# Performance work log

Measured on AMD Instinct MI355X. Metric: run time of the kernel, lower is better.

The kernel has to match this reference:

```python
import jax, jax.numpy as jnp
import numpy as np

QUERY_DIM = 1024
KEY_DIM = 768
NUM_HEADS = 16
HEAD_DIM = QUERY_DIM // NUM_HEADS


def _linear_params(key, in_dim, out_dim):
    kw, kb = jax.random.split(key)
    bound = 1.0 / np.sqrt(in_dim)
    W = jax.random.uniform(kw, (out_dim, in_dim), minval=-bound, maxval=bound, dtype=jnp.float32)
    b = jax.random.uniform(kb, (out_dim,), minval=-bound, maxval=bound, dtype=jnp.float32)
    return W, b


def setup_inputs() -> dict:
    key = jax.random.key(0)
    ks = jax.random.split(key, 7)
    B, Nq, Nk = 4, 1024, 2048
    query = jax.random.normal(ks[0], (B, Nq, QUERY_DIM), dtype=jnp.float32)
    k_in = jax.random.normal(ks[1], (B, Nk, KEY_DIM), dtype=jnp.float32)
    v_in = jax.random.normal(ks[2], (B, Nk, KEY_DIM), dtype=jnp.float32)
    Wq, bq = _linear_params(ks[3], QUERY_DIM, QUERY_DIM)
    Wk, bk = _linear_params(ks[4], KEY_DIM, QUERY_DIM)
    Wv, bv = _linear_params(ks[5], KEY_DIM, QUERY_DIM)
    Wo, bo = _linear_params(ks[6], QUERY_DIM, QUERY_DIM)
    return {
        "query": query, "key": k_in, "value": v_in,
        "Wq": Wq, "bq": bq, "Wk": Wk, "bk": bk,
        "Wv": Wv, "bv": bv, "Wo": Wo, "bo": bo,
    }


def reference(query, key, value, Wq, bq, Wk, bk, Wv, bv, Wo, bo):
    B, Nq, _ = query.shape
    Nk = key.shape[1]
    H, D = NUM_HEADS, HEAD_DIM
    scale = 1.0 / np.sqrt(D)
    # Projections (torch Linear: x @ W.T + b), then split heads -> (B, H, N, D)
    Q = (query @ Wq.T + bq).reshape(B, Nq, H, D).transpose(0, 2, 1, 3)
    K = (key @ Wk.T + bk).reshape(B, Nk, H, D).transpose(0, 2, 1, 3)
    V = (value @ Wv.T + bv).reshape(B, Nk, H, D).transpose(0, 2, 1, 3)
    # Explicit score matrix (B, H, Nq, Nk), softmax over keys
    attn = jnp.einsum('bhqd,bhkd->bhqk', Q, K) * scale
    attn = jax.nn.softmax(attn, axis=-1)
    out = jnp.einsum('bhqk,bhkd->bhqd', attn, V)
    out = out.transpose(0, 2, 1, 3).reshape(B, Nq, H * D)
    return out @ Wo.T + bo
```

## Files before the change

kernel.cpp:

```cpp
#include <hip/hip_runtime.h>
#include <stdint.h>


typedef __attribute__((ext_vector_type(4))) float f32x4;
typedef __attribute__((ext_vector_type(8))) _Float16 half8;
typedef __attribute__((ext_vector_type(4))) _Float16 half4;
typedef __attribute__((ext_vector_type(4))) short short4v;
typedef unsigned short u16;

__device__ __forceinline__ u16 f2h(float f){
  _Float16 h = (_Float16)f;
  return __builtin_bit_cast(unsigned short, h);
}

__device__ __forceinline__ void gload16(const void* g, void* lds){
  __builtin_amdgcn_global_load_lds((const __attribute__((address_space(1))) void*)g,
                                   (__attribute__((address_space(3))) void*)lds, 16, 0, 0);
}

struct Seg { const float* s; u16* d; int n4; };
struct Cvt7 { Seg seg[7]; };

__global__ __launch_bounds__(256) void cvt_f32_f16(Cvt7 a){
  Seg sg = a.seg[blockIdx.y];
  const long stride = (long)gridDim.x * 256;
  for (long i = (long)blockIdx.x*256 + threadIdx.x; i < sg.n4; i += stride){
    f32x4 v = *(const f32x4*)(sg.s + i*4);
    short4v h;
    h[0] = (short)f2h(v[0]); h[1] = (short)f2h(v[1]);
    h[2] = (short)f2h(v[2]); h[3] = (short)f2h(v[3]);
    *(short4v*)(sg.d + i*4) = h;
  }
}

template<int R>
__device__ __forceinline__ void stage_tile(const char* gbase, long gstride, char* lds, int tid){
  const int w = tid >> 6, lane = tid & 63;
  #pragma unroll
  for (int it = 0; it < R/32; ++it){
    int c  = (it*4 + w)*64 + lane;
    int r  = c >> 3;
    int bs = (c & 7) << 4;
    int sb = bs ^ ((r & 7) << 4);
    gload16(gbase + (long)r*gstride + sb, lds + (it*4 + w)*1024);
  }
}

template<int LAYOUT>
__global__ __launch_bounds__(256, 2)
void gemm_bt(const u16* __restrict__ A, const u16* __restrict__ Bt,
             const float* __restrict__ bias, u16* __restrict__ out16,
             float* __restrict__ outF, int K, int logS, float scale, int NkT)
{
  __shared__ __align__(128) char Alds[16384];
  __shared__ __align__(128) char Blds[16384];
  const int tid = threadIdx.x, lane = tid & 63, w = tid >> 6;
  const int g = lane >> 4, lm = lane & 15;
  const int row0 = blockIdx.x * 128, col0 = blockIdx.y * 128;
  const int wr = (w >> 1) * 64, wc = (w & 1) * 64;

  f32x4 acc[4][4];
  #pragma unroll
  for (int i = 0; i < 4; ++i)
    #pragma unroll
    for (int j = 0; j < 4; ++j) acc[i][j] = {0.f, 0.f, 0.f, 0.f};

  const char* Ag = (const char*)A  + ((long)row0 * K) * 2;
  const char* Bg = (const char*)Bt + ((long)col0 * K) * 2;

  for (int k0 = 0; k0 < K; k0 += 64){
    stage_tile<128>(Ag + k0*2, (long)K*2, Alds, tid);
    stage_tile<128>(Bg + k0*2, (long)K*2, Blds, tid);
    __syncthreads();
    #pragma unroll
    for (int kk = 0; kk < 2; ++kk){
      half8 af[4], bfr[4];
      #pragma unroll
      for (int mi = 0; mi < 4; ++mi){
        int r = wr + mi*16 + lm;
        af[mi] = *(const half8*)(Alds + r*128 + ((kk*64 + g*16) ^ ((r & 7) << 4)));
      }
      #pragma unroll
      for (int ni = 0; ni < 4; ++ni){
        int r = wc + ni*16 + lm;
        bfr[ni] = *(const half8*)(Blds + r*128 + ((kk*64 + g*16) ^ ((r & 7) << 4)));
      }
      #pragma unroll
      for (int mi = 0; mi < 4; ++mi)
        #pragma unroll
        for (int ni = 0; ni < 4; ++ni)
          acc[mi][ni] = __builtin_amdgcn_mfma_f32_16x16x32_f16(af[mi], bfr[ni], acc[mi][ni], 0, 0, 0);
    }
    __syncthreads();
  }

  float bv[4];
  #pragma unroll
  for (int ni = 0; ni < 4; ++ni) bv[ni] = bias[col0 + wc + ni*16 + lm];
  #pragma unroll
  for (int mi = 0; mi < 4; ++mi){
    #pragma unroll
    for (int ni = 0; ni < 4; ++ni){
      int n = col0 + wc + ni*16 + lm;
      #pragma unroll
      for (int r = 0; r < 4; ++r){
        int m = row0 + wr + mi*16 + g*4 + r;
        float v = (acc[mi][ni][r] + bv[ni]) * scale;
        if (LAYOUT == 3){
          outF[(long)m * 1024 + n] = v;
        } else {
          int b_ = m >> logS, s_ = m & ((1 << logS) - 1);
          int h_ = n >> 6,    d_ = n & 63;
          long dst;
          if (LAYOUT == 1) dst = (((long)(b_*16 + h_) << logS) + s_) * 64 + d_;
          else             dst = ((long)(b_*16 + h_) * 64 + d_) * (long)NkT + s_;
          out16[dst] = f2h(v);
        }
      }
    }
  }
}

__global__ __launch_bounds__(256, 2)
void attn_fused(const u16* __restrict__ Qw, const u16* __restrict__ Kw,
                const u16* __restrict__ Vtw, u16* __restrict__ AO)
{
  __shared__ __align__(128) char Klds[8192];
  __shared__ __align__(128) char Vlds[8192];
  const int tid = threadIdx.x, lane = tid & 63, w = tid >> 6;
  const int g = lane >> 4, lm = lane & 15;
  const int qt = blockIdx.x, bh = blockIdx.y;
  const long qbase = (long)bh * 1024 * 64;
  const long kbase = (long)bh * 2048 * 64;
  const long vbase = (long)bh * 64 * 2048;

  const int q0[2] = { qt*128 + w*32, qt*128 + w*32 + 16 };
  half8 aQ[2][2];
  #pragma unroll
  for (int s = 0; s < 2; ++s)
    #pragma unroll
    for (int kk = 0; kk < 2; ++kk)
      aQ[s][kk] = *(const half8*)((const char*)Qw + (qbase + (long)(q0[s] + lm)*64 + kk*32 + g*8)*2);

  float mrun[2] = {-3e38f, -3e38f};
  float lrun[2] = {0.f, 0.f};
  f32x4 O[2][4];
  #pragma unroll
  for (int s = 0; s < 2; ++s)
    #pragma unroll
    for (int di = 0; di < 4; ++di) O[s][di] = {0.f, 0.f, 0.f, 0.f};

  for (int kt = 0; kt < 2048; kt += 64){
    stage_tile<64>((const char*)Kw  + (kbase + (long)kt*64)*2, 128,  Klds, tid);
    stage_tile<64>((const char*)Vtw + (vbase + kt)*2,          4096, Vlds, tid);
    __syncthreads();

    half8 kf[4][2];
    #pragma unroll
    for (int t = 0; t < 4; ++t)
      #pragma unroll
      for (int kk = 0; kk < 2; ++kk){
        int r = t*16 + lm;
        kf[t][kk] = *(const half8*)(Klds + r*128 + ((kk*64 + g*16) ^ ((r & 7) << 4)));
      }

    #pragma unroll
    for (int s = 0; s < 2; ++s){
      f32x4 sc[4];
      #pragma unroll
      for (int t = 0; t < 4; ++t){
        f32x4 z = {0.f, 0.f, 0.f, 0.f};
        z = __builtin_amdgcn_mfma_f32_16x16x32_f16(kf[t][0], aQ[s][0], z, 0, 0, 0);
        z = __builtin_amdgcn_mfma_f32_16x16x32_f16(kf[t][1], aQ[s][1], z, 0, 0, 0);
        sc[t] = z;
      }
      float pm = sc[0][0];
      #pragma unroll
      for (int t = 0; t < 4; ++t)
        #pragma unroll
        for (int r = 0; r < 4; ++r) pm = fmaxf(pm, sc[t][r]);
      pm = fmaxf(pm, __shfl_xor(pm, 16));
      pm = fmaxf(pm, __shfl_xor(pm, 32));
      float mnew = fmaxf(mrun[s], pm);
      float fac  = __expf(mrun[s] - mnew);
      float ls = 0.f;
      #pragma unroll
      for (int t = 0; t < 4; ++t)
        #pragma unroll
        for (int r = 0; r < 4; ++r){ float p = __expf(sc[t][r] - mnew); sc[t][r] = p; ls += p; }
      ls += __shfl_xor(ls, 16);
      ls += __shfl_xor(ls, 32);
      lrun[s] = lrun[s]*fac + ls;
      mrun[s] = mnew;
      float frow[4];
      #pragma unroll
      for (int r = 0; r < 4; ++r) frow[r] = __shfl(fac, (lane & 48) | (g*4 + r));
      #pragma unroll
      for (int di = 0; di < 4; ++di){
        O[s][di][0] *= frow[0]; O[s][di][1] *= frow[1];
        O[s][di][2] *= frow[2]; O[s][di][3] *= frow[3];
      }
      half8 pa[2];
      #pragma unroll
      for (int kh = 0; kh < 2; ++kh)
        #pragma unroll
        for (int i = 0; i < 8; ++i){
          int t = kh*2 + (i >> 2), r = i & 3;
          pa[kh][i] = (_Float16)sc[t][r];
        }
      #pragma unroll
      for (int di = 0; di < 4; ++di){
        int d = di*16 + lm;
        int swz = (d & 7) << 4;
        #pragma unroll
        for (int kh = 0; kh < 2; ++kh){
          half4 lo = *(const half4*)(Vlds + d*128 + ((kh*64 + g*8)      ^ swz));
          half4 hi = *(const half4*)(Vlds + d*128 + ((kh*64 + g*8 + 32) ^ swz));
          half8 vf = { lo[0], lo[1], lo[2], lo[3], hi[0], hi[1], hi[2], hi[3] };
          O[s][di] = __builtin_amdgcn_mfma_f32_16x16x32_f16(pa[kh], vf, O[s][di], 0, 0, 0);
        }
      }
    }
    __syncthreads();
  }

  const int b = bh >> 4, h = bh & 15;
  #pragma unroll
  for (int s = 0; s < 2; ++s){
    float inv = 1.f / lrun[s];
    float irow[4];
    #pragma unroll
    for (int r = 0; r < 4; ++r) irow[r] = __shfl(inv, (lane & 48) | (g*4 + r));
    #pragma unroll
    for (int di = 0; di < 4; ++di)
      #pragma unroll
      for (int r = 0; r < 4; ++r){
        long q = q0[s] + g*4 + r;
        AO[((long)b*1024 + q)*1024 + h*64 + di*16 + lm] = f2h(O[s][di][r] * irow[r]);
      }
  }
}

extern "C" void kernel_launch(void* const* d_in, const int* in_sizes, int n_in,
                              void* d_out, int out_size, void* d_ws, size_t ws_size,
                              hipStream_t stream)
{
  const float* query = (const float*)d_in[0];
  const float* key   = (const float*)d_in[1];
  const float* value = (const float*)d_in[2];
  const float* Wq = (const float*)d_in[3];
  const float* bq = (const float*)d_in[4];
  const float* Wk = (const float*)d_in[5];
  const float* bk = (const float*)d_in[6];
  const float* Wv = (const float*)d_in[7];
  const float* bv = (const float*)d_in[8];
  const float* Wo = (const float*)d_in[9];
  const float* bo = (const float*)d_in[10];
  float* out = (float*)d_out;

  char* p = (char*)d_ws;
  auto alloc = [&](long bytes){ char* r = p; p += bytes; return r; };
  u16* qH  = (u16*)alloc( 8l<<20);
  u16* kH  = (u16*)alloc(12l<<20);
  u16* vH  = (u16*)alloc(12l<<20);
  u16* WqH = (u16*)alloc( 2l<<20);
  u16* WkH = (u16*)alloc( 2l<<20);
  u16* WvH = (u16*)alloc( 2l<<20);
  u16* WoH = (u16*)alloc( 2l<<20);
  u16* Qw  = (u16*)alloc( 8l<<20);
  u16* Kw  = (u16*)alloc(16l<<20);
  u16* Vtw = (u16*)alloc(16l<<20);
  u16* AO  = (u16*)alloc( 8l<<20);

  Cvt7 ca;
  ca.seg[0] = { query, qH,  4096*1024/4 };
  ca.seg[1] = { key,   kH,  8192*768/4  };
  ca.seg[2] = { value, vH,  8192*768/4  };
  ca.seg[3] = { Wq,    WqH, 1024*1024/4 };
  ca.seg[4] = { Wk,    WkH, 1024*768/4  };
  ca.seg[5] = { Wv,    WvH, 1024*768/4  };
  ca.seg[6] = { Wo,    WoH, 1024*1024/4 };
  cvt_f32_f16<<<dim3(512, 7), 256, 0, stream>>>(ca);

  dim3 blk(256);
  gemm_bt<1><<<dim3(32, 8), blk, 0, stream>>>(qH, WqH, bq, Qw,  nullptr, 1024, 10, 0.125f, 2048);
  gemm_bt<1><<<dim3(64, 8), blk, 0, stream>>>(kH, WkH, bk, Kw,  nullptr,  768, 11, 1.0f,   2048);
  gemm_bt<2><<<dim3(64, 8), blk, 0, stream>>>(vH, WvH, bv, Vtw, nullptr,  768, 11, 1.0f,   2048);
  attn_fused<<<dim3(8, 64), blk, 0, stream>>>(Qw, Kw, Vtw, AO);
  gemm_bt<3><<<dim3(32, 8), blk, 0, stream>>>(AO, WoH, bo, nullptr, out, 1024, 10, 1.0f, 2048);
}
```

Measured before the change: 278.7 us.

## Merge QKV projections into one launch, shrink GEMM tiles, widen attention blocks

Fuses the three Q/K/V projection GEMMs into a single kernel launch with 64x128 tiles, so each GEMM gets more blocks and more blocks can reside per CU. The V-transpose output is staged through LDS and written as 16-byte vectors instead of scattered 2-byte stores. The attention kernel now uses 512 threads with one 16-row query strip per wave, and the grid is remapped so blocks sharing a head are grouped. Each staged K/V tile is now shared by eight waves, but every wave does less work per tile, and the smaller GEMM tiles reload more operand data per output.

```diff
diff --git a/kernel.cpp b/kernel.cpp
--- a/kernel.cpp
+++ b/kernel.cpp
@@ -6,6 +6,7 @@
 typedef __attribute__((ext_vector_type(8))) _Float16 half8;
 typedef __attribute__((ext_vector_type(4))) _Float16 half4;
 typedef __attribute__((ext_vector_type(4))) short short4v;
+typedef __attribute__((ext_vector_type(8))) short short8;
 typedef unsigned short u16;
 
 __device__ __forceinline__ u16 f2h(float f){
@@ -33,95 +34,127 @@
   }
 }
 
-template<int R>
+template<int R, int THREADS>
 __device__ __forceinline__ void stage_tile(const char* gbase, long gstride, char* lds, int tid){
   const int w = tid >> 6, lane = tid & 63;
   #pragma unroll
-  for (int it = 0; it < R/32; ++it){
-    int c  = (it*4 + w)*64 + lane;
+  for (int it = 0; it < R*8/THREADS; ++it){
+    int c  = it*THREADS + w*64 + lane;
     int r  = c >> 3;
     int bs = (c & 7) << 4;
     int sb = bs ^ ((r & 7) << 4);
-    gload16(gbase + (long)r*gstride + sb, lds + (it*4 + w)*1024);
-  }
-}
-
-template<int LAYOUT>
-__global__ __launch_bounds__(256, 2)
-void gemm_bt(const u16* __restrict__ A, const u16* __restrict__ Bt,
-             const float* __restrict__ bias, u16* __restrict__ out16,
-             float* __restrict__ outF, int K, int logS, float scale, int NkT)
+    gload16(gbase + (long)r*gstride + sb, lds + (it*THREADS + w*64)*16);
+  }
+}
+
+__device__ __forceinline__ void gemm64_mainloop(const u16* A, const u16* Bt, int K,
+                                                int row0, int col0, int tid,
+                                                char* Alds, char* Blds, f32x4 acc[2][4]){
+  const int lane = tid & 63, w = tid >> 6;
+  const int g = lane >> 4, lm = lane & 15;
+  const int wr = (w >> 1) * 32, wc = (w & 1) * 64;
+  const char* Ag = (const char*)A  + ((long)row0 * K) * 2;
+  const char* Bg = (const char*)Bt + ((long)col0 * K) * 2;
+  for (int k0 = 0; k0 < K; k0 += 64){
+    stage_tile<64, 256>(Ag + k0*2, (long)K*2, Alds, tid);
+    stage_tile<128, 256>(Bg + k0*2, (long)K*2, Blds, tid);
+    __syncthreads();
+    #pragma unroll
+    for (int kk = 0; kk < 2; ++kk){
+      half8 af[2], bfr[4];
+      #pragma unroll
+      for (int mi = 0; mi < 2; ++mi){
+        int r = wr + mi*16 + lm;
+        af[mi] = *(const half8*)(Alds + r*128 + ((kk*64 + g*16) ^ ((r & 7) << 4)));
+      }
+      #pragma unroll
+      for (int ni = 0; ni < 4; ++ni){
+        int r = wc + ni*16 + lm;
+        bfr[ni] = *(const half8*)(Blds + r*128 + ((kk*64 + g*16) ^ ((r & 7) << 4)));
+      }
+      #pragma unroll
+      for (int mi = 0; mi < 2; ++mi)
+        #pragma unroll
+        for (int ni = 0; ni < 4; ++ni)
+          acc[mi][ni] = __builtin_amdgcn_mfma_f32_16x16x32_f16(af[mi], bfr[ni], acc[mi][ni], 0, 0, 0);
+    }
+    __syncthreads();
+  }
+}
+
+__global__ __launch_bounds__(256, 4)
+void qkv_proj(const u16* __restrict__ qH, const u16* __restrict__ kH, const u16* __restrict__ vH,
+              const u16* __restrict__ WqH, const u16* __restrict__ WkH, const u16* __restrict__ WvH,
+              const float* __restrict__ bq, const float* __restrict__ bk, const float* __restrict__ bv,
+              u16* __restrict__ Qw, u16* __restrict__ Kw, u16* __restrict__ Vtw)
 {
-  __shared__ __align__(128) char Alds[16384];
+  __shared__ __align__(128) char Alds[8192];
   __shared__ __align__(128) char Blds[16384];
   const int tid = threadIdx.x, lane = tid & 63, w = tid >> 6;
   const int g = lane >> 4, lm = lane & 15;
-  const int row0 = blockIdx.x * 128, col0 = blockIdx.y * 128;
-  const int wr = (w >> 1) * 64, wc = (w & 1) * 64;
-
-  f32x4 acc[4][4];
-  #pragma unroll
-  for (int i = 0; i < 4; ++i)
+
+  int bid = blockIdx.x;
+  const u16 *A, *Bt; const float* bias; u16* out16;
+  int K, logS, local; float scale = 1.0f;
+  int which;
+  if (bid < 512)       { which = 0; local = bid;        A = qH; Bt = WqH; bias = bq; out16 = Qw;  K = 1024; logS = 10; scale = 0.125f; }
+  else if (bid < 1536) { which = 1; local = bid - 512;  A = kH; Bt = WkH; bias = bk; out16 = Kw;  K = 768;  logS = 11; }
+  else                 { which = 2; local = bid - 1536; A = vH; Bt = WvH; bias = bv; out16 = Vtw; K = 768;  logS = 11; }
+  const int rb = local >> 3, cb = local & 7;
+  const int row0 = rb * 64, col0 = cb * 128;
+
+  f32x4 acc[2][4];
+  #pragma unroll
+  for (int i = 0; i < 2; ++i)
     #pragma unroll
     for (int j = 0; j < 4; ++j) acc[i][j] = {0.f, 0.f, 0.f, 0.f};
 
-  const char* Ag = (const char*)A  + ((long)row0 * K) * 2;
-  const char* Bg = (const char*)Bt + ((long)col0 * K) * 2;
-
-  for (int k0 = 0; k0 < K; k0 += 64){
-    stage_tile<128>(Ag + k0*2, (long)K*2, Alds, tid);
-    stage_tile<128>(Bg + k0*2, (long)K*2, Blds, tid);
-    __syncthreads();
-    #pragma unroll
-    for (int kk = 0; kk < 2; ++kk){
-      half8 af[4], bfr[4];
-      #pragma unroll
-      for (int mi = 0; mi < 4; ++mi){
-        int r = wr + mi*16 + lm;
-        af[mi] = *(const half8*)(Alds + r*128 + ((kk*64 + g*16) ^ ((r & 7) << 4)));
-      }
+  gemm64_mainloop(A, Bt, K, row0, col0, tid, Alds, Blds, acc);
+
+  const int wr = (w >> 1) * 32, wc = (w & 1) * 64;
+  if (which != 2){
+    #pragma unroll
+    for (int mi = 0; mi < 2; ++mi)
       #pragma unroll
       for (int ni = 0; ni < 4; ++ni){
-        int r = wc + ni*16 + lm;
-        bfr[ni] = *(const half8*)(Blds + r*128 + ((kk*64 + g*16) ^ ((r & 7) << 4)));
-      }
-      #pragma unroll
-      for (int mi = 0; mi < 4; ++mi)
+        int n = col0 + wc + ni*16 + lm;
+        float bvv = bias[n];
+        int h_ = n >> 6, d_ = n & 63;
         #pragma unroll
-        for (int ni = 0; ni < 4; ++ni)
-          acc[mi][ni] = __builtin_amdgcn_mfma_f32_16x16x32_f16(af[mi], bfr[ni], acc[mi][ni], 0, 0, 0);
-    }
-    __syncthreads();
-  }
-
-  float bv[4];
-  #pragma unroll
-  for (int ni = 0; ni < 4; ++ni) bv[ni] = bias[col0 + wc + ni*16 + lm];
-  #pragma unroll
-  for (int mi = 0; mi < 4; ++mi){
-    #pragma unroll
-    for (int ni = 0; ni < 4; ++ni){
-      int n = col0 + wc + ni*16 + lm;
-      #pragma unroll
-      for (int r = 0; r < 4; ++r){
-        int m = row0 + wr + mi*16 + g*4 + r;
-        float v = (acc[mi][ni][r] + bv[ni]) * scale;
-        if (LAYOUT == 3){
-          outF[(long)m * 1024 + n] = v;
-        } else {
+        for (int r = 0; r < 4; ++r){
+          int m = row0 + wr + mi*16 + g*4 + r;
           int b_ = m >> logS, s_ = m & ((1 << logS) - 1);
-          int h_ = n >> 6,    d_ = n & 63;
-          long dst;
-          if (LAYOUT == 1) dst = (((long)(b_*16 + h_) << logS) + s_) * 64 + d_;
-          else             dst = ((long)(b_*16 + h_) * 64 + d_) * (long)NkT + s_;
-          out16[dst] = f2h(v);
+          long dst = (((long)(b_*16 + h_) << logS) + s_) * 64 + d_;
+          out16[dst] = f2h((acc[mi][ni][r] + bvv) * scale);
         }
       }
-    }
-  }
-}
-
-__global__ __launch_bounds__(256, 2)
+  } else {
+    #pragma unroll
+    for (int mi = 0; mi < 2; ++mi)
+      #pragma unroll
+      for (int ni = 0; ni < 4; ++ni){
+        int np = wc + ni*16 + lm;
+        float bvv = bias[col0 + np];
+        short4v h4;
+        #pragma unroll
+        for (int r = 0; r < 4; ++r) h4[r] = (short)f2h(acc[mi][ni][r] + bvv);
+        int mb = (wr + mi*16 + g*4) * 2;
+        *(short4v*)(Blds + np*128 + (mb ^ ((np & 7) << 4))) = h4;
+      }
+    __syncthreads();
+    const int b_ = row0 >> 11;
+    #pragma unroll
+    for (int pass = 0; pass < 4; ++pass){
+      int idx = pass*256 + tid, row = idx >> 3, c = idx & 7;
+      short8 v = *(const short8*)(Blds + row*128 + ((c*16) ^ ((row & 7) << 4)));
+      int ng = col0 + row, h_ = ng >> 6, d_ = ng & 63;
+      long dst = ((long)(b_*16 + h_)*64 + d_)*2048 + (row0 & 2047) + c*8;
+      *(short8*)(out16 + dst) = v;
+    }
+  }
+}
+
+__global__ __launch_bounds__(512, 4)
 void attn_fused(const u16* __restrict__ Qw, const u16* __restrict__ Kw,
                 const u16* __restrict__ Vtw, u16* __restrict__ AO)
 {
@@ -129,30 +162,28 @@
   __shared__ __align__(128) char Vlds[8192];
   const int tid = threadIdx.x, lane = tid & 63, w = tid >> 6;
   const int g = lane >> 4, lm = lane & 15;
-  const int qt = blockIdx.x, bh = blockIdx.y;
+  const int p = blockIdx.x;
+  const int slot = p >> 3;
+  const int bh = (p & 7) + ((slot & 7) << 3);
+  const int qt = slot >> 3;
   const long qbase = (long)bh * 1024 * 64;
   const long kbase = (long)bh * 2048 * 64;
   const long vbase = (long)bh * 64 * 2048;
 
-  const int q0[2] = { qt*128 + w*32, qt*128 + w*32 + 16 };
-  half8 aQ[2][2];
-  #pragma unroll
-  for (int s = 0; s < 2; ++s)
-    #pragma unroll
-    for (int kk = 0; kk < 2; ++kk)
-      aQ[s][kk] = *(const half8*)((const char*)Qw + (qbase + (long)(q0[s] + lm)*64 + kk*32 + g*8)*2);
-
-  float mrun[2] = {-3e38f, -3e38f};
-  float lrun[2] = {0.f, 0.f};
-  f32x4 O[2][4];
-  #pragma unroll
-  for (int s = 0; s < 2; ++s)
-    #pragma unroll
-    for (int di = 0; di < 4; ++di) O[s][di] = {0.f, 0.f, 0.f, 0.f};
+  const int q0 = qt*128 + w*16;
+  half8 aQ[2];
+  #pragma unroll
+  for (int kk = 0; kk < 2; ++kk)
+    aQ[kk] = *(const half8*)((const char*)Qw + (qbase + (long)(q0 + lm)*64 + kk*32 + g*8)*2);
+
+  float mrun = -3e38f, lrun = 0.f;
+  f32x4 O[4];
+  #pragma unroll
+  for (int di = 0; di < 4; ++di) O[di] = {0.f, 0.f, 0.f, 0.f};
 
   for (int kt = 0; kt < 2048; kt += 64){
-    stage_tile<64>((const char*)Kw  + (kbase + (long)kt*64)*2, 128,  Klds, tid);
-    stage_tile<64>((const char*)Vtw + (vbase + kt)*2,          4096, Vlds, tid);
+    stage_tile<64, 512>((const char*)Kw  + (kbase + (long)kt*64)*2, 128,  Klds, tid);
+    stage_tile<64, 512>((const char*)Vtw + (vbase + kt)*2,          4096, Vlds, tid);
     __syncthreads();
 
     half8 kf[4][2];
@@ -164,81 +195,109 @@
         kf[t][kk] = *(const half8*)(Klds + r*128 + ((kk*64 + g*16) ^ ((r & 7) << 4)));
       }
 
-    #pragma unroll
-    for (int s = 0; s < 2; ++s){
-      f32x4 sc[4];
-      #pragma unroll
-      for (int t = 0; t < 4; ++t){
-        f32x4 z = {0.f, 0.f, 0.f, 0.f};
-        z = __builtin_amdgcn_mfma_f32_16x16x32_f16(kf[t][0], aQ[s][0], z, 0, 0, 0);
-        z = __builtin_amdgcn_mfma_f32_16x16x32_f16(kf[t][1], aQ[s][1], z, 0, 0, 0);
-        sc[t] = z;
-      }
-      float pm = sc[0][0];
-      #pragma unroll
-      for (int t = 0; t < 4; ++t)
-        #pragma unroll
-        for (int r = 0; r < 4; ++r) pm = fmaxf(pm, sc[t][r]);
-      pm = fmaxf(pm, __shfl_xor(pm, 16));
-      pm = fmaxf(pm, __shfl_xor(pm, 32));
-      float mnew = fmaxf(mrun[s], pm);
-      float fac  = __expf(mrun[s] - mnew);
-      float ls = 0.f;
-      #pragma unroll
-      for (int t = 0; t < 4; ++t)
-        #pragma unroll
-        for (int r = 0; r < 4; ++r){ float p = __expf(sc[t][r] - mnew); sc[t][r] = p; ls += p; }
-      ls += __shfl_xor(ls, 16);
-      ls += __shfl_xor(ls, 32);
-      lrun[s] = lrun[s]*fac + ls;
-      mrun[s] = mnew;
-      float frow[4];
-      #pragma unroll
-      for (int r = 0; r < 4; ++r) frow[r] = __shfl(fac, (lane & 48) | (g*4 + r));
-      #pragma unroll
-      for (int di = 0; di < 4; ++di){
-        O[s][di][0] *= frow[0]; O[s][di][1] *= frow[1];
-        O[s][di][2] *= frow[2]; O[s][di][3] *= frow[3];
-      }
-      half8 pa[2];
-      #pragma unroll
-      for (int kh = 0; kh < 2; ++kh)
-        #pragma unroll
-        for (int i = 0; i < 8; ++i){
-          int t = kh*2 + (i >> 2), r = i & 3;
-          pa[kh][i] = (_Float16)sc[t][r];
-        }
-      #pragma unroll
-      for (int di = 0; di < 4; ++di){
-        int d = di*16 + lm;
-        int swz = (d & 7) << 4;
-        #pragma unroll
-        for (int kh = 0; kh < 2; ++kh){
-          half4 lo = *(const half4*)(Vlds + d*128 + ((kh*64 + g*8)      ^ swz));
-          half4 hi = *(const half4*)(Vlds + d*128 + ((kh*64 + g*8 + 32) ^ swz));
-          half8 vf = { lo[0], lo[1], lo[2], lo[3], hi[0], hi[1], hi[2], hi[3] };
-          O[s][di] = __builtin_amdgcn_mfma_f32_16x16x32_f16(pa[kh], vf, O[s][di], 0, 0, 0);
-        }
+    f32x4 sc[4];
+    #pragma unroll
+    for (int t = 0; t < 4; ++t){
+      f32x4 z = {0.f, 0.f, 0.f, 0.f};
+      z = __builtin_amdgcn_mfma_f32_16x16x32_f16(kf[t][0], aQ[0], z, 0, 0, 0);
+      z = __builtin_amdgcn_mfma_f32_16x16x32_f16(kf[t][1], aQ[1], z, 0, 0, 0);
+      sc[t] = z;
+    }
+    float pm = sc[0][0];
+    #pragma unroll
+    for (int t = 0; t < 4; ++t)
+      #pragma unroll
+      for (int r = 0; r < 4; ++r) pm = fmaxf(pm, sc[t][r]);
+    pm = fmaxf(pm, __shfl_xor(pm, 16));
+    pm = fmaxf(pm, __shfl_xor(pm, 32));
+    float mnew = fmaxf(mrun, pm);
+    float fac  = __expf(mrun - mnew);
+    float ls = 0.f;
+    #pragma unroll
+    for (int t = 0; t < 4; ++t)
+      #pragma unroll
+      for (int r = 0; r < 4; ++r){ float pv = __expf(sc[t][r] - mnew); sc[t][r] = pv; ls += pv; }
+    ls += __shfl_xor(ls, 16);
+    ls += __shfl_xor(ls, 32);
+    lrun = lrun*fac + ls;
+    mrun = mnew;
+    float frow[4];
+    #pragma unroll
+    for (int r = 0; r < 4; ++r) frow[r] = __shfl(fac, (lane & 48) | (g*4 + r));
+    #pragma unroll
+    for (int di = 0; di < 4; ++di){
+      O[di][0] *= frow[0]; O[di][1] *= frow[1];
+      O[di][2] *= frow[2]; O[di][3] *= frow[3];
+    }
+    half8 pa[2];
+    #pragma unroll
+    for (int kh = 0; kh < 2; ++kh)
+      #pragma unroll
+      for (int i = 0; i < 8; ++i){
+        int t = kh*2 + (i >> 2), r = i & 3;
+        pa[kh][i] = (_Float16)sc[t][r];
+      }
+    #pragma unroll
+    for (int di = 0; di < 4; ++di){
+      int d = di*16 + lm;
+      int swz = (d & 7) << 4;
+      #pragma unroll
+      for (int kh = 0; kh < 2; ++kh){
+        half4 lo = *(const half4*)(Vlds + d*128 + ((kh*64 + g*8)      ^ swz));
+        half4 hi = *(const half4*)(Vlds + d*128 + ((kh*64 + g*8 + 32) ^ swz));
+        half8 vf = { lo[0], lo[1], lo[2], lo[3], hi[0], hi[1], hi[2], hi[3] };
+        O[di] = __builtin_amdgcn_mfma_f32_16x16x32_f16(pa[kh], vf, O[di], 0, 0, 0);
       }
     }
     __syncthreads();
   }
 
   const int b = bh >> 4, h = bh & 15;
-  #pragma unroll
-  for (int s = 0; s < 2; ++s){
-    float inv = 1.f / lrun[s];
-    float irow[4];
-    #pragma unroll
-    for (int r = 0; r < 4; ++r) irow[r] = __shfl(inv, (lane & 48) | (g*4 + r));
-    #pragma unroll
-    for (int di = 0; di < 4; ++di)
+  float inv = 1.f / lrun;
+  float irow[4];
+  #pragma unroll
+  for (int r = 0; r < 4; ++r) irow[r] = __shfl(inv, (lane & 48) | (g*4 + r));
+  #pragma unroll
+  for (int di = 0; di < 4; ++di)
+    #pragma unroll
+    for (int r = 0; r < 4; ++r){
+      long q = q0 + g*4 + r;
+      AO[((long)b*1024 + q)*1024 + h*64 + di*16 + lm] = f2h(O[di][r] * irow[r]);
+    }
+}
+
+__global__ __launch_bounds__(256, 4)
+void gemm_o(const u16* __restrict__ A, const u16* __restrict__ Bt,
+            const float* __restrict__ bias, float* __restrict__ outF)
+{
+  __shared__ __align__(128) char Alds[8192];
+  __shared__ __align__(128) char Blds[16384];
+  const int tid = threadIdx.x, lane = tid & 63, w = tid >> 6;
+  const int g = lane >> 4, lm = lane & 15;
+  const int rb = blockIdx.x >> 3, cb = blockIdx.x & 7;
+  const int row0 = rb * 64, col0 = cb * 128;
+
+  f32x4 acc[2][4];
+  #pragma unroll
+  for (int i = 0; i < 2; ++i)
+    #pragma unroll
+    for (int j = 0; j < 4; ++j) acc[i][j] = {0.f, 0.f, 0.f, 0.f};
+
+  gemm64_mainloop(A, Bt, 1024, row0, col0, tid, Alds, Blds, acc);
+
+  const int wr = (w >> 1) * 32, wc = (w & 1) * 64;
+  #pragma unroll
+  for (int mi = 0; mi < 2; ++mi)
+    #pragma unroll
+    for (int ni = 0; ni < 4; ++ni){
+      int n = col0 + wc + ni*16 + lm;
+      float bvv = bias[n];
       #pragma unroll
       for (int r = 0; r < 4; ++r){
-        long q = q0[s] + g*4 + r;
-        AO[((long)b*1024 + q)*1024 + h*64 + di*16 + lm] = f2h(O[s][di][r] * irow[r]);
-      }
-  }
+        int m = row0 + wr + mi*16 + g*4 + r;
+        outF[(long)m * 1024 + n] = acc[mi][ni][r] + bvv;
+      }
+    }
 }
 
 extern "C" void kernel_launch(void* const* d_in, const int* in_sizes, int n_in,
@@ -282,10 +341,8 @@
   ca.seg[6] = { Wo,    WoH, 1024*1024/4 };
   cvt_f32_f16<<<dim3(512, 7), 256, 0, stream>>>(ca);
 
-  dim3 blk(256);
-  gemm_bt<1><<<dim3(32, 8), blk, 0, stream>>>(qH, WqH, bq, Qw,  nullptr, 1024, 10, 0.125f, 2048);
-  gemm_bt<1><<<dim3(64, 8), blk, 0, stream>>>(kH, WkH, bk, Kw,  nullptr,  768, 11, 1.0f,   2048);
-  gemm_bt<2><<<dim3(64, 8), blk, 0, stream>>>(vH, WvH, bv, Vtw, nullptr,  768, 11, 1.0f,   2048);
-  attn_fused<<<dim3(8, 64), blk, 0, stream>>>(Qw, Kw, Vtw, AO);
-  gemm_bt<3><<<dim3(32, 8), blk, 0, stream>>>(AO, WoH, bo, nullptr, out, 1024, 10, 1.0f, 2048);
-}
+  qkv_proj<<<dim3(2560), dim3(256), 0, stream>>>(qH, kH, vH, WqH, WkH, WvH,
+                                                 bq, bk, bv, Qw, Kw, Vtw);
+  attn_fused<<<dim3(512), dim3(512), 0, stream>>>(Qw, Kw, Vtw, AO);
+  gemm_o<<<dim3(512), dim3(256), 0, stream>>>(AO, WoH, bo, out);
+}
```

Result: faster. 267.6 us (-4.0%).
